# Optimization experiments

Measured on AMD Instinct MI355X. Metric: run time of the kernel, lower is better.

Reference implementation:

```python
import jax, jax.numpy as jnp
import numpy as np

N_NODES = 100000
N_EDGES = 1200000
D_IN = 64
D_HID = 64


def _sage_conv(x, src, dst, W_l, W_r, b, num_nodes):
    # PyG SAGEConv (mean aggr): out = mean_{j in N(i)} x_j @ W_l^T + x_i @ W_r^T + b
    msgs = x[src]                                                   # [E, d] gather
    summed = jax.ops.segment_sum(msgs, dst, num_segments=num_nodes)  # [N, d] scatter-add
    cnt = jax.ops.segment_sum(jnp.ones((src.shape[0],), x.dtype), dst,
                              num_segments=num_nodes)                # [N]
    agg = summed / jnp.maximum(cnt, 1.0)[:, None]                    # mean, safe for isolated nodes
    return agg @ W_l.T + x @ W_r.T + b


def setup_inputs() -> dict:
    key = jax.random.key(0)
    ks = jax.random.split(key, 8)
    x = jax.random.normal(ks[0], (N_NODES, D_IN), dtype=jnp.float32)
    edge_index = jax.random.randint(ks[1], (2, N_EDGES), 0, N_NODES, dtype=jnp.int32)
    s = 1.0 / np.sqrt(D_IN)
    W1_l = jax.random.uniform(ks[2], (D_HID, D_IN), jnp.float32, -s, s)
    W1_r = jax.random.uniform(ks[3], (D_HID, D_IN), jnp.float32, -s, s)
    b1 = jnp.zeros((D_HID,), jnp.float32)
    s2 = 1.0 / np.sqrt(D_HID)
    W2_l = jax.random.uniform(ks[4], (D_HID, D_HID), jnp.float32, -s2, s2)
    W2_r = jax.random.uniform(ks[5], (D_HID, D_HID), jnp.float32, -s2, s2)
    b2 = jnp.zeros((D_HID,), jnp.float32)
    return {"x": x, "edge_index": edge_index, "W1_l": W1_l, "W1_r": W1_r, "b1": b1,
            "W2_l": W2_l, "W2_r": W2_r, "b2": b2}


def reference(x, edge_index, W1_l, W1_r, b1, W2_l, W2_r, b2):
    src, dst = edge_index[0], edge_index[1]  # messages flow src -> dst
    n = x.shape[0]
    h = _sage_conv(x, src, dst, W1_l, W1_r, b1, n)
    h = jax.nn.relu(h)  # dropout is identity in eval mode
    h = _sage_conv(h, src, dst, W2_l, W2_r, b2, n)
    return h
```

## Files before the change

kernel.cpp:

```cpp
#include <hip/hip_runtime.h>
#include <hip/hip_fp16.h>

#define NN 100000
#define NE 1200000
#define D 64
#define TBM 64
#define NBK 391
#define BSH 8
#define BMSK 255
#define CAP 4096

__global__ __launch_bounds__(256) void k_prep(const float* __restrict__ in,
                                              __half* __restrict__ outh, int n8,
                                              int* __restrict__ cur) {
  int i = blockIdx.x * 256 + threadIdx.x;
  if (i < 512) cur[i] = 0;
  if (i >= n8) return;
  float4 a = ((const float4*)in)[2 * i];
  float4 b = ((const float4*)in)[2 * i + 1];
  union { __half2 h; unsigned u; } p0, p1, p2, p3;
  p0.h = __floats2half2_rn(a.x, a.y);
  p1.h = __floats2half2_rn(a.z, a.w);
  p2.h = __floats2half2_rn(b.x, b.y);
  p3.h = __floats2half2_rn(b.z, b.w);
  uint4 o = {p0.u, p1.u, p2.u, p3.u};
  ((uint4*)outh)[i] = o;
}

__global__ __launch_bounds__(256) void k_bin(const int* __restrict__ src,
                                             const int* __restrict__ dst,
                                             int* __restrict__ cur,
                                             int* __restrict__ eidx, int E) {
  __shared__ int lhist[NBK];
  __shared__ int lbase[NBK];
  int tid = threadIdx.x;
  int chunk = (E + gridDim.x - 1) / gridDim.x;
  int e0 = blockIdx.x * chunk;
  int e1 = min(e0 + chunk, E);

  for (int i = tid; i < NBK; i += 256) lhist[i] = 0;
  __syncthreads();
  for (int e = e0 + tid; e < e1; e += 256) atomicAdd(&lhist[dst[e] >> BSH], 1);
  __syncthreads();
  for (int i = tid; i < NBK; i += 256) {
    int c = lhist[i];
    lbase[i] = c ? atomicAdd(&cur[i], c) : 0;
  }
  __syncthreads();
  for (int i = tid; i < NBK; i += 256) lhist[i] = 0;
  __syncthreads();
  for (int e = e0 + tid; e < e1; e += 256) {
    int d = dst[e];
    int b = d >> BSH;
    int r = atomicAdd(&lhist[b], 1);
    int p = lbase[b] + r;
    if (p < CAP) eidx[b * CAP + p] = ((d & BMSK) << 20) | src[e];
  }
}

__global__ __launch_bounds__(256) void k_sort(int* __restrict__ eidx,
                                              const int* __restrict__ cur,
                                              int* __restrict__ off,
                                              int* __restrict__ deg, int N) {
  __shared__ int recS[CAP];
  __shared__ int srtS[CAP];
  __shared__ int hist[256];
  __shared__ int scan[256];
  __shared__ int cursor[256];

  int b = blockIdx.x;
  int tid = threadIdx.x;
  int cnt = min(cur[b], CAP);
  int ebase = b * CAP;

  for (int i = tid; i < cnt; i += 256) recS[i] = eidx[ebase + i];
  hist[tid] = 0;
  __syncthreads();
  for (int i = tid; i < cnt; i += 256) atomicAdd(&hist[recS[i] >> 20], 1);
  __syncthreads();

  int v = hist[tid];
  scan[tid] = v;
  __syncthreads();
  for (int o = 1; o < 256; o <<= 1) {
    int add = (tid >= o) ? scan[tid - o] : 0;
    __syncthreads();
    scan[tid] += add;
    __syncthreads();
  }
  int excl = scan[tid] - v;
  cursor[tid] = excl;
  __syncthreads();

  for (int i = tid; i < cnt; i += 256) {
    int rec = recS[i];
    int p = atomicAdd(&cursor[rec >> 20], 1);
    srtS[p] = rec & 0xFFFFF;
  }
  __syncthreads();
  for (int i = tid; i < cnt; i += 256) eidx[ebase + i] = srtS[i];

  int node = (b << BSH) + tid;
  if (node < N) {
    off[node] = ebase + excl;
    deg[node] = v;
  }
}

template <int RELU, int OUTH>
__global__ __launch_bounds__(256, 4) void sage_layer(
    const __half* __restrict__ feat,
    const int* __restrict__ off,
    const int* __restrict__ deg,
    const int* __restrict__ eidx,
    const float* __restrict__ Wl,
    const float* __restrict__ Wr,
    const float* __restrict__ bias,
    void* __restrict__ outp,
    int N) {
  __shared__ __align__(16) float At[TBM * 68];
  __shared__ __align__(16) float Wt[64 * 68];

  int tid = threadIdx.x;
  int tx = tid & 15;
  int ty = tid >> 4;
  int base = blockIdx.x * TBM;

  {
    int g = tid >> 2;
    int lane = tid & 3;
    int node = base + g;
    float a0 = 0.f, a1 = 0.f, a2 = 0.f, a3 = 0.f;
    float a4 = 0.f, a5 = 0.f, a6 = 0.f, a7 = 0.f;
    float a8 = 0.f, a9 = 0.f, aA = 0.f, aB = 0.f;
    float aC = 0.f, aD = 0.f, aE = 0.f, aF = 0.f;
    if (node < N) {
      int start = off[node];
      int cnt = deg[node];
      const uint4* f4 = (const uint4*)feat;
      union { unsigned x; __half2 h; } c;
      float2 t;
      int j = 0;
#pragma unroll 2
      for (; j + 2 <= cnt; j += 2) {
        int s0 = eidx[start + j];
        int s1 = eidx[start + j + 1];
        uint4 u0 = f4[(size_t)s0 * 8 + lane * 2];
        uint4 u1 = f4[(size_t)s0 * 8 + lane * 2 + 1];
        uint4 v0 = f4[(size_t)s1 * 8 + lane * 2];
        uint4 v1 = f4[(size_t)s1 * 8 + lane * 2 + 1];
        c.x = u0.x; t = __half22float2(c.h); a0 += t.x; a1 += t.y;
        c.x = u0.y; t = __half22float2(c.h); a2 += t.x; a3 += t.y;
        c.x = u0.z; t = __half22float2(c.h); a4 += t.x; a5 += t.y;
        c.x = u0.w; t = __half22float2(c.h); a6 += t.x; a7 += t.y;
        c.x = u1.x; t = __half22float2(c.h); a8 += t.x; a9 += t.y;
        c.x = u1.y; t = __half22float2(c.h); aA += t.x; aB += t.y;
        c.x = u1.z; t = __half22float2(c.h); aC += t.x; aD += t.y;
        c.x = u1.w; t = __half22float2(c.h); aE += t.x; aF += t.y;
        c.x = v0.x; t = __half22float2(c.h); a0 += t.x; a1 += t.y;
        c.x = v0.y; t = __half22float2(c.h); a2 += t.x; a3 += t.y;
        c.x = v0.z; t = __half22float2(c.h); a4 += t.x; a5 += t.y;
        c.x = v0.w; t = __half22float2(c.h); a6 += t.x; a7 += t.y;
        c.x = v1.x; t = __half22float2(c.h); a8 += t.x; a9 += t.y;
        c.x = v1.y; t = __half22float2(c.h); aA += t.x; aB += t.y;
        c.x = v1.z; t = __half22float2(c.h); aC += t.x; aD += t.y;
        c.x = v1.w; t = __half22float2(c.h); aE += t.x; aF += t.y;
      }
      if (j < cnt) {
        int s0 = eidx[start + j];
        uint4 u0 = f4[(size_t)s0 * 8 + lane * 2];
        uint4 u1 = f4[(size_t)s0 * 8 + lane * 2 + 1];
        c.x = u0.x; t = __half22float2(c.h); a0 += t.x; a1 += t.y;
        c.x = u0.y; t = __half22float2(c.h); a2 += t.x; a3 += t.y;
        c.x = u0.z; t = __half22float2(c.h); a4 += t.x; a5 += t.y;
        c.x = u0.w; t = __half22float2(c.h); a6 += t.x; a7 += t.y;
        c.x = u1.x; t = __half22float2(c.h); a8 += t.x; a9 += t.y;
        c.x = u1.y; t = __half22float2(c.h); aA += t.x; aB += t.y;
        c.x = u1.z; t = __half22float2(c.h); aC += t.x; aD += t.y;
        c.x = u1.w; t = __half22float2(c.h); aE += t.x; aF += t.y;
      }
      float inv = 1.0f / fmaxf((float)cnt, 1.0f);
      a0 *= inv; a1 *= inv; a2 *= inv; a3 *= inv;
      a4 *= inv; a5 *= inv; a6 *= inv; a7 *= inv;
      a8 *= inv; a9 *= inv; aA *= inv; aB *= inv;
      aC *= inv; aD *= inv; aE *= inv; aF *= inv;
    }
    float* dst = At + g * 68 + lane * 16;
    *(float4*)(dst + 0)  = make_float4(a0, a1, a2, a3);
    *(float4*)(dst + 4)  = make_float4(a4, a5, a6, a7);
    *(float4*)(dst + 8)  = make_float4(a8, a9, aA, aB);
    *(float4*)(dst + 12) = make_float4(aC, aD, aE, aF);
  }
#pragma unroll 1
  for (int i = 0; i < 4; ++i) {
    int f = tid + 256 * i;
    int k = f & 63;
    int n4 = f >> 6;
    float4 w;
    w.x = Wl[(4 * n4 + 0) * D + k];
    w.y = Wl[(4 * n4 + 1) * D + k];
    w.z = Wl[(4 * n4 + 2) * D + k];
    w.w = Wl[(4 * n4 + 3) * D + k];
    *(float4*)(Wt + k * 68 + 4 * n4) = w;
  }
  __syncthreads();

  float acc[4][4];
#pragma unroll
  for (int i = 0; i < 4; ++i)
#pragma unroll
    for (int j = 0; j < 4; ++j) acc[i][j] = 0.f;

#pragma unroll 2
  for (int kq = 0; kq < 16; ++kq) {
    float4 a0 = *(const float4*)(At + (4 * ty + 0) * 68 + 4 * kq);
    float4 a1 = *(const float4*)(At + (4 * ty + 1) * 68 + 4 * kq);
    float4 a2 = *(const float4*)(At + (4 * ty + 2) * 68 + 4 * kq);
    float4 a3 = *(const float4*)(At + (4 * ty + 3) * 68 + 4 * kq);
    float4 w0 = *(const float4*)(Wt + (4 * kq + 0) * 68 + 4 * tx);
    float4 w1 = *(const float4*)(Wt + (4 * kq + 1) * 68 + 4 * tx);
    float4 w2 = *(const float4*)(Wt + (4 * kq + 2) * 68 + 4 * tx);
    float4 w3 = *(const float4*)(Wt + (4 * kq + 3) * 68 + 4 * tx);
#define ROW(i, a)                                                      \
    acc[i][0] += a.x * w0.x; acc[i][1] += a.x * w0.y;                  \
    acc[i][2] += a.x * w0.z; acc[i][3] += a.x * w0.w;                  \
    acc[i][0] += a.y * w1.x; acc[i][1] += a.y * w1.y;                  \
    acc[i][2] += a.y * w1.z; acc[i][3] += a.y * w1.w;                  \
    acc[i][0] += a.z * w2.x; acc[i][1] += a.z * w2.y;                  \
    acc[i][2] += a.z * w2.z; acc[i][3] += a.z * w2.w;                  \
    acc[i][0] += a.w * w3.x; acc[i][1] += a.w * w3.y;                  \
    acc[i][2] += a.w * w3.z; acc[i][3] += a.w * w3.w;
    ROW(0, a0) ROW(1, a1) ROW(2, a2) ROW(3, a3)
  }
  __syncthreads();

#pragma unroll 1
  for (int i = 0; i < 4; ++i) {
    int f = tid + 256 * i;
    int row = f >> 4;
    int c4 = f & 15;
    int node = base + row;
    float4 v = make_float4(0.f, 0.f, 0.f, 0.f);
    if (node < N) {
      uint2 u = ((const uint2*)feat)[(size_t)node * 16 + c4];
      union { unsigned x; __half2 h; } c;
      c.x = u.x; float2 f0 = __half22float2(c.h);
      c.x = u.y; float2 f1 = __half22float2(c.h);
      v = make_float4(f0.x, f0.y, f1.x, f1.y);
    }
    *(float4*)(At + row * 68 + 4 * c4) = v;
  }
#pragma unroll 1
  for (int i = 0; i < 4; ++i) {
    int f = tid + 256 * i;
    int k = f & 63;
    int n4 = f >> 6;
    float4 w;
    w.x = Wr[(4 * n4 + 0) * D + k];
    w.y = Wr[(4 * n4 + 1) * D + k];
    w.z = Wr[(4 * n4 + 2) * D + k];
    w.w = Wr[(4 * n4 + 3) * D + k];
    *(float4*)(Wt + k * 68 + 4 * n4) = w;
  }
  __syncthreads();

#pragma unroll 2
  for (int kq = 0; kq < 16; ++kq) {
    float4 a0 = *(const float4*)(At + (4 * ty + 0) * 68 + 4 * kq);
    float4 a1 = *(const float4*)(At + (4 * ty + 1) * 68 + 4 * kq);
    float4 a2 = *(const float4*)(At + (4 * ty + 2) * 68 + 4 * kq);
    float4 a3 = *(const float4*)(At + (4 * ty + 3) * 68 + 4 * kq);
    float4 w0 = *(const float4*)(Wt + (4 * kq + 0) * 68 + 4 * tx);
    float4 w1 = *(const float4*)(Wt + (4 * kq + 1) * 68 + 4 * tx);
    float4 w2 = *(const float4*)(Wt + (4 * kq + 2) * 68 + 4 * tx);
    float4 w3 = *(const float4*)(Wt + (4 * kq + 3) * 68 + 4 * tx);
    ROW(0, a0) ROW(1, a1) ROW(2, a2) ROW(3, a3)
#undef ROW
  }

  float4 bv = ((const float4*)bias)[tx];
#pragma unroll
  for (int i = 0; i < 4; ++i) {
    int node = base + 4 * ty + i;
    if (node < N) {
      float4 o;
      o.x = acc[i][0] + bv.x;
      o.y = acc[i][1] + bv.y;
      o.z = acc[i][2] + bv.z;
      o.w = acc[i][3] + bv.w;
      if (RELU) {
        o.x = fmaxf(o.x, 0.f); o.y = fmaxf(o.y, 0.f);
        o.z = fmaxf(o.z, 0.f); o.w = fmaxf(o.w, 0.f);
      }
      if (OUTH) {
        union { __half2 h; unsigned u; } p0, p1;
        p0.h = __floats2half2_rn(o.x, o.y);
        p1.h = __floats2half2_rn(o.z, o.w);
        uint2 ov = {p0.u, p1.u};
        ((uint2*)outp)[(size_t)node * 16 + tx] = ov;
      } else {
        ((float4*)outp)[(size_t)node * 16 + tx] = o;
      }
    }
  }
}

extern "C" void kernel_launch(void* const* d_in, const int* in_sizes, int n_in,
                              void* d_out, int out_size, void* d_ws, size_t ws_size,
                              hipStream_t stream) {
  const float* x   = (const float*)d_in[0];
  const int* edge  = (const int*)d_in[1];
  const float* W1l = (const float*)d_in[2];
  const float* W1r = (const float*)d_in[3];
  const float* b1  = (const float*)d_in[4];
  const float* W2l = (const float*)d_in[5];
  const float* W2r = (const float*)d_in[6];
  const float* b2  = (const float*)d_in[7];
  float* out = (float*)d_out;

  const int N = NN, E = NE;
  const int* src = edge;
  const int* dst = edge + E;

  int* cur    = (int*)d_ws;
  int* eidx   = cur + 512;
  int* off    = eidx + (size_t)NBK * CAP;
  int* deg    = off + N;
  __half* x_h = (__half*)(deg + N);
  __half* h_h = x_h + (size_t)N * D;

  const int gridT = (N + TBM - 1) / TBM;
  const int gridC = (N * D / 8 + 255) / 256;

  k_prep<<<gridC, 256, 0, stream>>>(x, x_h, N * D / 8, cur);
  k_bin<<<768, 256, 0, stream>>>(src, dst, cur, eidx, E);
  k_sort<<<NBK, 256, 0, stream>>>(eidx, cur, off, deg, N);

  sage_layer<1, 1><<<gridT, 256, 0, stream>>>(x_h, off, deg, eidx,
                                              W1l, W1r, b1, h_h, N);
  sage_layer<0, 0><<<gridT, 256, 0, stream>>>(h_h, off, deg, eidx,
                                              W2l, W2r, b2, out, N);
}
```

Before: 137.2 us.

## Split feature gather into sliced layout kernel separate from dense matmul

Features are stored in four 16-column slices (slice-major), so each gather block touches one 3.2MB slice that can stay cache-resident, with one thread per node gathering 32 bytes per neighbor. Aggregation moves into its own kernel that writes an fp16 mean buffer, and the transform kernel reads it back and does both matmuls in one loop. The cost is an extra global round-trip of the aggregate, extra launches, and eidx being read four times, all in exchange for better L2 locality on the random gathers.

```diff
diff --git a/kernel.cpp b/kernel.cpp
--- a/kernel.cpp
+++ b/kernel.cpp
@@ -9,22 +9,29 @@
 #define BSH 8
 #define BMSK 255
 #define CAP 4096
+#define NSL 4
+
 
 __global__ __launch_bounds__(256) void k_prep(const float* __restrict__ in,
-                                              __half* __restrict__ outh, int n8,
+                                              __half* __restrict__ xs, int N,
                                               int* __restrict__ cur) {
   int i = blockIdx.x * 256 + threadIdx.x;
   if (i < 512) cur[i] = 0;
-  if (i >= n8) return;
-  float4 a = ((const float4*)in)[2 * i];
-  float4 b = ((const float4*)in)[2 * i + 1];
+  if (i >= N * 8) return;
+  int q = i / (N * 2);
+  int j = i - q * N * 2;
+  int node = j >> 1;
+  int half = j & 1;
+  const float* src = in + (size_t)node * D + q * 16 + half * 8;
+  float4 a = *(const float4*)(src);
+  float4 b = *(const float4*)(src + 4);
   union { __half2 h; unsigned u; } p0, p1, p2, p3;
   p0.h = __floats2half2_rn(a.x, a.y);
   p1.h = __floats2half2_rn(a.z, a.w);
   p2.h = __floats2half2_rn(b.x, b.y);
   p3.h = __floats2half2_rn(b.z, b.w);
   uint4 o = {p0.u, p1.u, p2.u, p3.u};
-  ((uint4*)outh)[i] = o;
+  ((uint4*)xs)[(size_t)(q * N + node) * 2 + half] = o;
 }
 
 __global__ __launch_bounds__(256) void k_bin(const int* __restrict__ src,
@@ -107,12 +114,85 @@
   }
 }
 
+__global__ __launch_bounds__(256) void k_gather(const __half* __restrict__ feat_s,
+                                                const int* __restrict__ off,
+                                                const int* __restrict__ deg,
+                                                const int* __restrict__ eidx,
+                                                __half* __restrict__ agg, int N) {
+  int q = blockIdx.x & 3;
+  int b = blockIdx.x >> 2;
+  int node = (b << BSH) + threadIdx.x;
+  if (node >= N) return;
+  int start = off[node];
+  int cnt = deg[node];
+  const uint4* f4 = (const uint4*)feat_s + (size_t)q * N * 2;
+
+  float a0 = 0.f, a1 = 0.f, a2 = 0.f, a3 = 0.f;
+  float a4 = 0.f, a5 = 0.f, a6 = 0.f, a7 = 0.f;
+  float a8 = 0.f, a9 = 0.f, aA = 0.f, aB = 0.f;
+  float aC = 0.f, aD = 0.f, aE = 0.f, aF = 0.f;
+  union { unsigned x; __half2 h; } c;
+  float2 t;
+  int j = 0;
+#pragma unroll 2
+  for (; j + 2 <= cnt; j += 2) {
+    int s0 = eidx[start + j];
+    int s1 = eidx[start + j + 1];
+    uint4 u0 = f4[(size_t)s0 * 2];
+    uint4 u1 = f4[(size_t)s0 * 2 + 1];
+    uint4 v0 = f4[(size_t)s1 * 2];
+    uint4 v1 = f4[(size_t)s1 * 2 + 1];
+    c.x = u0.x; t = __half22float2(c.h); a0 += t.x; a1 += t.y;
+    c.x = u0.y; t = __half22float2(c.h); a2 += t.x; a3 += t.y;
+    c.x = u0.z; t = __half22float2(c.h); a4 += t.x; a5 += t.y;
+    c.x = u0.w; t = __half22float2(c.h); a6 += t.x; a7 += t.y;
+    c.x = u1.x; t = __half22float2(c.h); a8 += t.x; a9 += t.y;
+    c.x = u1.y; t = __half22float2(c.h); aA += t.x; aB += t.y;
+    c.x = u1.z; t = __half22float2(c.h); aC += t.x; aD += t.y;
+    c.x = u1.w; t = __half22float2(c.h); aE += t.x; aF += t.y;
+    c.x = v0.x; t = __half22float2(c.h); a0 += t.x; a1 += t.y;
+    c.x = v0.y; t = __half22float2(c.h); a2 += t.x; a3 += t.y;
+    c.x = v0.z; t = __half22float2(c.h); a4 += t.x; a5 += t.y;
+    c.x = v0.w; t = __half22float2(c.h); a6 += t.x; a7 += t.y;
+    c.x = v1.x; t = __half22float2(c.h); a8 += t.x; a9 += t.y;
+    c.x = v1.y; t = __half22float2(c.h); aA += t.x; aB += t.y;
+    c.x = v1.z; t = __half22float2(c.h); aC += t.x; aD += t.y;
+    c.x = v1.w; t = __half22float2(c.h); aE += t.x; aF += t.y;
+  }
+  if (j < cnt) {
+    int s0 = eidx[start + j];
+    uint4 u0 = f4[(size_t)s0 * 2];
+    uint4 u1 = f4[(size_t)s0 * 2 + 1];
+    c.x = u0.x; t = __half22float2(c.h); a0 += t.x; a1 += t.y;
+    c.x = u0.y; t = __half22float2(c.h); a2 += t.x; a3 += t.y;
+    c.x = u0.z; t = __half22float2(c.h); a4 += t.x; a5 += t.y;
+    c.x = u0.w; t = __half22float2(c.h); a6 += t.x; a7 += t.y;
+    c.x = u1.x; t = __half22float2(c.h); a8 += t.x; a9 += t.y;
+    c.x = u1.y; t = __half22float2(c.h); aA += t.x; aB += t.y;
+    c.x = u1.z; t = __half22float2(c.h); aC += t.x; aD += t.y;
+    c.x = u1.w; t = __half22float2(c.h); aE += t.x; aF += t.y;
+  }
+  float inv = 1.0f / fmaxf((float)cnt, 1.0f);
+  union { __half2 h; unsigned u; } p0, p1, p2, p3;
+  p0.h = __floats2half2_rn(a0 * inv, a1 * inv);
+  p1.h = __floats2half2_rn(a2 * inv, a3 * inv);
+  p2.h = __floats2half2_rn(a4 * inv, a5 * inv);
+  p3.h = __floats2half2_rn(a6 * inv, a7 * inv);
+  uint4 o0 = {p0.u, p1.u, p2.u, p3.u};
+  p0.h = __floats2half2_rn(a8 * inv, a9 * inv);
+  p1.h = __floats2half2_rn(aA * inv, aB * inv);
+  p2.h = __floats2half2_rn(aC * inv, aD * inv);
+  p3.h = __floats2half2_rn(aE * inv, aF * inv);
+  uint4 o1 = {p0.u, p1.u, p2.u, p3.u};
+  uint4* ap = (uint4*)agg + (size_t)node * 8 + q * 2;
+  ap[0] = o0;
+  ap[1] = o1;
+}
+
 template <int RELU, int OUTH>
-__global__ __launch_bounds__(256, 4) void sage_layer(
-    const __half* __restrict__ feat,
-    const int* __restrict__ off,
-    const int* __restrict__ deg,
-    const int* __restrict__ eidx,
+__global__ __launch_bounds__(256, 4) void sage_mm(
+    const __half* __restrict__ aggh,
+    const __half* __restrict__ feat_s,
     const float* __restrict__ Wl,
     const float* __restrict__ Wr,
     const float* __restrict__ bias,
@@ -126,156 +206,75 @@
   int ty = tid >> 4;
   int base = blockIdx.x * TBM;
 
-  {
-    int g = tid >> 2;
-    int lane = tid & 3;
-    int node = base + g;
-    float a0 = 0.f, a1 = 0.f, a2 = 0.f, a3 = 0.f;
-    float a4 = 0.f, a5 = 0.f, a6 = 0.f, a7 = 0.f;
-    float a8 = 0.f, a9 = 0.f, aA = 0.f, aB = 0.f;
-    float aC = 0.f, aD = 0.f, aE = 0.f, aF = 0.f;
-    if (node < N) {
-      int start = off[node];
-      int cnt = deg[node];
-      const uint4* f4 = (const uint4*)feat;
-      union { unsigned x; __half2 h; } c;
-      float2 t;
-      int j = 0;
-#pragma unroll 2
-      for (; j + 2 <= cnt; j += 2) {
-        int s0 = eidx[start + j];
-        int s1 = eidx[start + j + 1];
-        uint4 u0 = f4[(size_t)s0 * 8 + lane * 2];
-        uint4 u1 = f4[(size_t)s0 * 8 + lane * 2 + 1];
-        uint4 v0 = f4[(size_t)s1 * 8 + lane * 2];
-        uint4 v1 = f4[(size_t)s1 * 8 + lane * 2 + 1];
-        c.x = u0.x; t = __half22float2(c.h); a0 += t.x; a1 += t.y;
-        c.x = u0.y; t = __half22float2(c.h); a2 += t.x; a3 += t.y;
-        c.x = u0.z; t = __half22float2(c.h); a4 += t.x; a5 += t.y;
-        c.x = u0.w; t = __half22float2(c.h); a6 += t.x; a7 += t.y;
-        c.x = u1.x; t = __half22float2(c.h); a8 += t.x; a9 += t.y;
-        c.x = u1.y; t = __half22float2(c.h); aA += t.x; aB += t.y;
-        c.x = u1.z; t = __half22float2(c.h); aC += t.x; aD += t.y;
-        c.x = u1.w; t = __half22float2(c.h); aE += t.x; aF += t.y;
-        c.x = v0.x; t = __half22float2(c.h); a0 += t.x; a1 += t.y;
-        c.x = v0.y; t = __half22float2(c.h); a2 += t.x; a3 += t.y;
-        c.x = v0.z; t = __half22float2(c.h); a4 += t.x; a5 += t.y;
-        c.x = v0.w; t = __half22float2(c.h); a6 += t.x; a7 += t.y;
-        c.x = v1.x; t = __half22float2(c.h); a8 += t.x; a9 += t.y;
-        c.x = v1.y; t = __half22float2(c.h); aA += t.x; aB += t.y;
-        c.x = v1.z; t = __half22float2(c.h); aC += t.x; aD += t.y;
-        c.x = v1.w; t = __half22float2(c.h); aE += t.x; aF += t.y;
-      }
-      if (j < cnt) {
-        int s0 = eidx[start + j];
-        uint4 u0 = f4[(size_t)s0 * 8 + lane * 2];
-        uint4 u1 = f4[(size_t)s0 * 8 + lane * 2 + 1];
-        c.x = u0.x; t = __half22float2(c.h); a0 += t.x; a1 += t.y;
-        c.x = u0.y; t = __half22float2(c.h); a2 += t.x; a3 += t.y;
-        c.x = u0.z; t = __half22float2(c.h); a4 += t.x; a5 += t.y;
-        c.x = u0.w; t = __half22float2(c.h); a6 += t.x; a7 += t.y;
-        c.x = u1.x; t = __half22float2(c.h); a8 += t.x; a9 += t.y;
-        c.x = u1.y; t = __half22float2(c.h); aA += t.x; aB += t.y;
-        c.x = u1.z; t = __half22float2(c.h); aC += t.x; aD += t.y;
-        c.x = u1.w; t = __half22float2(c.h); aE += t.x; aF += t.y;
-      }
-      float inv = 1.0f / fmaxf((float)cnt, 1.0f);
-      a0 *= inv; a1 *= inv; a2 *= inv; a3 *= inv;
-      a4 *= inv; a5 *= inv; a6 *= inv; a7 *= inv;
-      a8 *= inv; a9 *= inv; aA *= inv; aB *= inv;
-      aC *= inv; aD *= inv; aE *= inv; aF *= inv;
-    }
-    float* dst = At + g * 68 + lane * 16;
-    *(float4*)(dst + 0)  = make_float4(a0, a1, a2, a3);
-    *(float4*)(dst + 4)  = make_float4(a4, a5, a6, a7);
-    *(float4*)(dst + 8)  = make_float4(a8, a9, aA, aB);
-    *(float4*)(dst + 12) = make_float4(aC, aD, aE, aF);
-  }
-#pragma unroll 1
-  for (int i = 0; i < 4; ++i) {
-    int f = tid + 256 * i;
-    int k = f & 63;
-    int n4 = f >> 6;
-    float4 w;
-    w.x = Wl[(4 * n4 + 0) * D + k];
-    w.y = Wl[(4 * n4 + 1) * D + k];
-    w.z = Wl[(4 * n4 + 2) * D + k];
-    w.w = Wl[(4 * n4 + 3) * D + k];
-    *(float4*)(Wt + k * 68 + 4 * n4) = w;
-  }
-  __syncthreads();
-
   float acc[4][4];
 #pragma unroll
   for (int i = 0; i < 4; ++i)
 #pragma unroll
     for (int j = 0; j < 4; ++j) acc[i][j] = 0.f;
 
+#pragma unroll 1
+  for (int ph = 0; ph < 2; ++ph) {
+    const float* W = ph ? Wr : Wl;
+    if (ph) __syncthreads();
+
+#pragma unroll 1
+    for (int i = 0; i < 4; ++i) {
+      int f = tid + 256 * i;
+      int row = f >> 4;
+      int c4 = f & 15;
+      int node = base + row;
+      float4 v = make_float4(0.f, 0.f, 0.f, 0.f);
+      if (node < N) {
+        uint2 u;
+        if (ph == 0) {
+          u = ((const uint2*)aggh)[(size_t)node * 16 + c4];
+        } else {
+          int q = c4 >> 2;
+          u = ((const uint2*)feat_s)[(size_t)(q * N + node) * 4 + (c4 & 3)];
+        }
+        union { unsigned x; __half2 h; } c;
+        c.x = u.x; float2 f0 = __half22float2(c.h);
+        c.x = u.y; float2 f1 = __half22float2(c.h);
+        v = make_float4(f0.x, f0.y, f1.x, f1.y);
+      }
+      *(float4*)(At + row * 68 + 4 * c4) = v;
+    }
+#pragma unroll 1
+    for (int i = 0; i < 4; ++i) {
+      int f = tid + 256 * i;
+      int k = f & 63;
+      int n4 = f >> 6;
+      float4 w;
+      w.x = W[(4 * n4 + 0) * D + k];
+      w.y = W[(4 * n4 + 1) * D + k];
+      w.z = W[(4 * n4 + 2) * D + k];
+      w.w = W[(4 * n4 + 3) * D + k];
+      *(float4*)(Wt + k * 68 + 4 * n4) = w;
+    }
+    __syncthreads();
+
 #pragma unroll 2
-  for (int kq = 0; kq < 16; ++kq) {
-    float4 a0 = *(const float4*)(At + (4 * ty + 0) * 68 + 4 * kq);
-    float4 a1 = *(const float4*)(At + (4 * ty + 1) * 68 + 4 * kq);
-    float4 a2 = *(const float4*)(At + (4 * ty + 2) * 68 + 4 * kq);
-    float4 a3 = *(const float4*)(At + (4 * ty + 3) * 68 + 4 * kq);
-    float4 w0 = *(const float4*)(Wt + (4 * kq + 0) * 68 + 4 * tx);
-    float4 w1 = *(const float4*)(Wt + (4 * kq + 1) * 68 + 4 * tx);
-    float4 w2 = *(const float4*)(Wt + (4 * kq + 2) * 68 + 4 * tx);
-    float4 w3 = *(const float4*)(Wt + (4 * kq + 3) * 68 + 4 * tx);
+    for (int kq = 0; kq < 16; ++kq) {
+      float4 a0 = *(const float4*)(At + (4 * ty + 0) * 68 + 4 * kq);
+      float4 a1 = *(const float4*)(At + (4 * ty + 1) * 68 + 4 * kq);
+      float4 a2 = *(const float4*)(At + (4 * ty + 2) * 68 + 4 * kq);
+      float4 a3 = *(const float4*)(At + (4 * ty + 3) * 68 + 4 * kq);
+      float4 w0 = *(const float4*)(Wt + (4 * kq + 0) * 68 + 4 * tx);
+      float4 w1 = *(const float4*)(Wt + (4 * kq + 1) * 68 + 4 * tx);
+      float4 w2 = *(const float4*)(Wt + (4 * kq + 2) * 68 + 4 * tx);
+      float4 w3 = *(const float4*)(Wt + (4 * kq + 3) * 68 + 4 * tx);
 #define ROW(i, a)                                                      \
-    acc[i][0] += a.x * w0.x; acc[i][1] += a.x * w0.y;                  \
-    acc[i][2] += a.x * w0.z; acc[i][3] += a.x * w0.w;                  \
-    acc[i][0] += a.y * w1.x; acc[i][1] += a.y * w1.y;                  \
-    acc[i][2] += a.y * w1.z; acc[i][3] += a.y * w1.w;                  \
-    acc[i][0] += a.z * w2.x; acc[i][1] += a.z * w2.y;                  \
-    acc[i][2] += a.z * w2.z; acc[i][3] += a.z * w2.w;                  \
-    acc[i][0] += a.w * w3.x; acc[i][1] += a.w * w3.y;                  \
-    acc[i][2] += a.w * w3.z; acc[i][3] += a.w * w3.w;
-    ROW(0, a0) ROW(1, a1) ROW(2, a2) ROW(3, a3)
-  }
-  __syncthreads();
-
-#pragma unroll 1
-  for (int i = 0; i < 4; ++i) {
-    int f = tid + 256 * i;
-    int row = f >> 4;
-    int c4 = f & 15;
-    int node = base + row;
-    float4 v = make_float4(0.f, 0.f, 0.f, 0.f);
-    if (node < N) {
-      uint2 u = ((const uint2*)feat)[(size_t)node * 16 + c4];
-      union { unsigned x; __half2 h; } c;
-      c.x = u.x; float2 f0 = __half22float2(c.h);
-      c.x = u.y; float2 f1 = __half22float2(c.h);
-      v = make_float4(f0.x, f0.y, f1.x, f1.y);
+      acc[i][0] += a.x * w0.x; acc[i][1] += a.x * w0.y;                \
+      acc[i][2] += a.x * w0.z; acc[i][3] += a.x * w0.w;                \
+      acc[i][0] += a.y * w1.x; acc[i][1] += a.y * w1.y;                \
+      acc[i][2] += a.y * w1.z; acc[i][3] += a.y * w1.w;                \
+      acc[i][0] += a.z * w2.x; acc[i][1] += a.z * w2.y;                \
+      acc[i][2] += a.z * w2.z; acc[i][3] += a.z * w2.w;                \
+      acc[i][0] += a.w * w3.x; acc[i][1] += a.w * w3.y;                \
+      acc[i][2] += a.w * w3.z; acc[i][3] += a.w * w3.w;
+      ROW(0, a0) ROW(1, a1) ROW(2, a2) ROW(3, a3)
+#undef ROW
     }
-    *(float4*)(At + row * 68 + 4 * c4) = v;
-  }
-#pragma unroll 1
-  for (int i = 0; i < 4; ++i) {
-    int f = tid + 256 * i;
-    int k = f & 63;
-    int n4 = f >> 6;
-    float4 w;
-    w.x = Wr[(4 * n4 + 0) * D + k];
-    w.y = Wr[(4 * n4 + 1) * D + k];
-    w.z = Wr[(4 * n4 + 2) * D + k];
-    w.w = Wr[(4 * n4 + 3) * D + k];
-    *(float4*)(Wt + k * 68 + 4 * n4) = w;
-  }
-  __syncthreads();
-
-#pragma unroll 2
-  for (int kq = 0; kq < 16; ++kq) {
-    float4 a0 = *(const float4*)(At + (4 * ty + 0) * 68 + 4 * kq);
-    float4 a1 = *(const float4*)(At + (4 * ty + 1) * 68 + 4 * kq);
-    float4 a2 = *(const float4*)(At + (4 * ty + 2) * 68 + 4 * kq);
-    float4 a3 = *(const float4*)(At + (4 * ty + 3) * 68 + 4 * kq);
-    float4 w0 = *(const float4*)(Wt + (4 * kq + 0) * 68 + 4 * tx);
-    float4 w1 = *(const float4*)(Wt + (4 * kq + 1) * 68 + 4 * tx);
-    float4 w2 = *(const float4*)(Wt + (4 * kq + 2) * 68 + 4 * tx);
-    float4 w3 = *(const float4*)(Wt + (4 * kq + 3) * 68 + 4 * tx);
-    ROW(0, a0) ROW(1, a1) ROW(2, a2) ROW(3, a3)
-#undef ROW
   }
 
   float4 bv = ((const float4*)bias)[tx];
@@ -297,7 +296,8 @@
         p0.h = __floats2half2_rn(o.x, o.y);
         p1.h = __floats2half2_rn(o.z, o.w);
         uint2 ov = {p0.u, p1.u};
-        ((uint2*)outp)[(size_t)node * 16 + tx] = ov;
+        int q = tx >> 2;
+        ((uint2*)outp)[(size_t)(q * N + node) * 4 + (tx & 3)] = ov;
       } else {
         ((float4*)outp)[(size_t)node * 16 + tx] = o;
       }
@@ -322,22 +322,25 @@
   const int* src = edge;
   const int* dst = edge + E;
 
-  int* cur    = (int*)d_ws;
-  int* eidx   = cur + 512;
-  int* off    = eidx + (size_t)NBK * CAP;
-  int* deg    = off + N;
-  __half* x_h = (__half*)(deg + N);
-  __half* h_h = x_h + (size_t)N * D;
+  int* cur      = (int*)d_ws;
+  int* eidx     = cur + 512;
+  int* off      = eidx + (size_t)NBK * CAP;
+  int* deg      = off + N;
+  __half* x_s   = (__half*)(deg + N);
+  __half* h_s   = x_s + (size_t)N * D;
+  __half* agg_h = h_s + (size_t)N * D;
 
   const int gridT = (N + TBM - 1) / TBM;
-  const int gridC = (N * D / 8 + 255) / 256;
-
-  k_prep<<<gridC, 256, 0, stream>>>(x, x_h, N * D / 8, cur);
+  const int gridP = (N * 8 + 255) / 256;
+  const int gridG = NBK * 4;
+
+  k_prep<<<gridP, 256, 0, stream>>>(x, x_s, N, cur);
   k_bin<<<768, 256, 0, stream>>>(src, dst, cur, eidx, E);
   k_sort<<<NBK, 256, 0, stream>>>(eidx, cur, off, deg, N);
 
-  sage_layer<1, 1><<<gridT, 256, 0, stream>>>(x_h, off, deg, eidx,
-                                              W1l, W1r, b1, h_h, N);
-  sage_layer<0, 0><<<gridT, 256, 0, stream>>>(h_h, off, deg, eidx,
-                                              W2l, W2r, b2, out, N);
-}
+  k_gather<<<gridG, 256, 0, stream>>>(x_s, off, deg, eidx, agg_h, N);
+  sage_mm<1, 1><<<gridT, 256, 0, stream>>>(agg_h, x_s, W1l, W1r, b1, h_s, N);
+
+  k_gather<<<gridG, 256, 0, stream>>>(h_s, off, deg, eidx, agg_h, N);
+  sage_mm<0, 0><<<gridT, 256, 0, stream>>>(agg_h, h_s, W2l, W2r, b2, out, N);
+}
```

After: 213.2 us. 55.4% more time.
